# Kernel optimization log

Hardware: AMD Instinct MI355X
Metric: run time of the kernel (lower is better)

Reference implementation:

```python
import jax, jax.numpy as jnp
import numpy as np

EPS = 1e-5  # torch BatchNorm1d default eps


def setup_inputs() -> dict:
    key = jax.random.key(0)
    ks = jax.random.split(key, 4)
    B, D, H, T = 1024, 256, 1024, 128
    s_ih = 1.0 / np.sqrt(H)
    return {
        "x": jax.random.normal(ks[0], (B, D), dtype=jnp.float32),
        "h0": jnp.zeros((B, H), dtype=jnp.float32),
        "W_ih": jax.random.normal(ks[1], (3 * H, D), dtype=jnp.float32) * s_ih,
        "W_hh": jax.random.normal(ks[2], (3 * H, H), dtype=jnp.float32) * s_ih,
        "b_ih": jnp.zeros((3 * H,), dtype=jnp.float32),
        "b_hh": jnp.zeros((3 * H,), dtype=jnp.float32),
        "W_lin": jax.random.normal(ks[3], (D, H), dtype=jnp.float32) * s_ih,
        "b_lin": jnp.zeros((D,), dtype=jnp.float32),
        "n_frames": T,
    }


def reference(x, h0, W_ih, W_hh, b_ih, b_hh, W_lin, b_lin, n_frames):
    H = h0.shape[-1]

    def step(carry, _):
        h, inp = carry
        gi = inp @ W_ih.T + b_ih          # (B, 3H)
        gh = h @ W_hh.T + b_hh            # (B, 3H)
        i_r, i_z, i_n = jnp.split(gi, 3, axis=-1)
        h_r, h_z, h_n = jnp.split(gh, 3, axis=-1)
        r = jax.nn.sigmoid(i_r + h_r)
        z = jax.nn.sigmoid(i_z + h_z)
        n = jnp.tanh(i_n + r * h_n)
        h_new = (1.0 - z) * n + z * h
        out = h_new @ W_lin.T + b_lin     # (B, D) -> next input
        return (h_new, out), out

    _, outs = jax.lax.scan(step, (h0, x), None, length=n_frames)  # (T, B, D)

    # BatchNorm1d(affine=False), training mode: per-frame batch statistics
    mean = outs.mean(axis=1, keepdims=True)
    var = outs.var(axis=1, keepdims=True)  # biased variance, as torch BN uses
    return (outs - mean) * jax.lax.rsqrt(var + EPS)
```

## Files before the change

### kernel.cpp

```cpp
#include <hip/hip_runtime.h>


#define DEVI __device__ __forceinline__

typedef __bf16 bf16x8 __attribute__((ext_vector_type(8)));
typedef float f32x4 __attribute__((ext_vector_type(4)));
typedef unsigned int u32x4 __attribute__((ext_vector_type(4)));

typedef __attribute__((address_space(1))) const unsigned int g_u32;
typedef __attribute__((address_space(3))) unsigned int l_u32;

DEVI unsigned short f2b(float f) {
  union { float f; unsigned u; } v; v.f = f;
  return (unsigned short)((v.u + 0x7fffu + ((v.u >> 16) & 1u)) >> 16);
}

DEVI void gl_lds16(const void* g, void* s) {
  __builtin_amdgcn_global_load_lds((g_u32*)g, (l_u32*)s, 16, 0, 0);
}
DEVI void st16_sc1(void* p, u32x4 v) {
  asm volatile("global_store_dwordx4 %0, %1, off sc1"
               :: "v"((unsigned long long)(__SIZE_TYPE__)p), "v"(v) : "memory");
}

DEVI float sigm(float x) { return 1.0f / (1.0f + __expf(-x)); }
DEVI float tanh_f(float x) {
  float t = __expf(-2.0f * fabsf(x));
  float r = (1.0f - t) / (1.0f + t);
  return x >= 0.0f ? r : -r;
}

__global__ __launch_bounds__(256, 2) void gru_persist(
    const unsigned short* __restrict__ XB,
    const unsigned short* __restrict__ WP0,
    const unsigned short* __restrict__ WP,
    const float* __restrict__ C0v,
    const float* __restrict__ CBv,
    const float* __restrict__ h0,
    unsigned short* __restrict__ HH,
    unsigned int* __restrict__ bar)
{
  __shared__ __align__(16) unsigned short As[3][64 * 64];
  __shared__ __align__(16) unsigned short Bs[3][128 * 64];
  __shared__ __align__(16) unsigned short Hs[64 * 32];
  const int tid = threadIdx.x;
  const int w = tid >> 6, lane = tid & 63;
  const int wr = w >> 1, wc = w & 1;
  const int srow = lane >> 3;
  const int schunk = (lane & 7) ^ srow;
  const int l15 = lane & 15, lg = lane >> 4;
  const int xb_ = blockIdx.x & 7, rb_ = blockIdx.x >> 3;
  const int mb = (xb_ >> 2) | ((rb_ & 7) << 1);
  const int nb = (xb_ & 3) | ((rb_ >> 3) << 2);
  const int j = nb * 32 + wc * 16 + l15;

  const float c0r = C0v[j], c0z = C0v[1024 + j], c0i = C0v[2048 + j], c0h = C0v[3072 + j];
  const float cbr = CBv[j], cbz = CBv[1024 + j], cbi = CBv[2048 + j], cbh = CBv[3072 + j];

  float hreg[2][4];
#pragma unroll
  for (int mi = 0; mi < 2; ++mi)
#pragma unroll
    for (int i = 0; i < 4; ++i)
      hreg[mi][i] = h0[(size_t)(mb * 64 + wr * 32 + mi * 16 + lg * 4 + i) * 1024 + j];

  int offA[2][2], offB[2][4];
#pragma unroll
  for (int kk = 0; kk < 2; ++kk) {
#pragma unroll
    for (int mi = 0; mi < 2; ++mi) {
      int rl = wr * 32 + mi * 16 + l15;
      int slot = (kk * 4 + lg) ^ (rl & 7);
      offA[kk][mi] = rl * 128 + slot * 16;
    }
#pragma unroll
    for (int g = 0; g < 4; ++g) {
      int cl = wc * 64 + g * 16 + l15;
      int slot = (kk * 4 + lg) ^ (cl & 7);
      offB[kk][g] = cl * 128 + slot * 16;
    }
  }
  const int offq0 = srow * 1024 + schunk * 8;
  const int offq1 = (8 + srow) * 1024 + schunk * 8;
  const int offq2 = (16 + srow) * 1024 + schunk * 8;
  const int offq3 = (24 + srow) * 1024 + schunk * 8;
  const size_t arow_off = (size_t)(mb * 64 + w * 16) * 1024;
  const unsigned short* BrowS = WP + (size_t)(nb * 128 + w * 32) * 1024;
  const unsigned short* Arow0 = XB + (size_t)(mb * 64 + w * 16) * 256;
  const unsigned short* Brow0 = WP0 + (size_t)(nb * 128 + w * 32) * 256;

#define STAGE0(KT, BUF)                                                       \
  _Pragma("unroll")                                                           \
  for (int q = 0; q < 4; ++q)                                                 \
    gl_lds16(Brow0 + (size_t)(q * 8 + srow) * 256 + (KT) * 64 + schunk * 8,   \
             (char*)Bs[BUF] + (w * 32 + q * 8) * 128);                        \
  _Pragma("unroll")                                                           \
  for (int q = 0; q < 2; ++q)                                                 \
    gl_lds16(Arow0 + (size_t)(q * 8 + srow) * 256 + (KT) * 64 + schunk * 8,   \
             (char*)As[BUF] + (w * 16 + q * 8) * 128);
#define SSTAGE_B(KT, BUF)                                                     \
  gl_lds16(BrowS + offq0 + (KT) * 64, (char*)Bs[BUF] + (w * 32) * 128);       \
  gl_lds16(BrowS + offq1 + (KT) * 64, (char*)Bs[BUF] + (w * 32 + 8) * 128);   \
  gl_lds16(BrowS + offq2 + (KT) * 64, (char*)Bs[BUF] + (w * 32 + 16) * 128);  \
  gl_lds16(BrowS + offq3 + (KT) * 64, (char*)Bs[BUF] + (w * 32 + 24) * 128);
#define SSTAGE_A(KT, BUF)                                                     \
  gl_lds16(ArowS + offq0 + (KT) * 64, (char*)As[BUF] + (w * 16) * 128);       \
  gl_lds16(ArowS + offq1 + (KT) * 64, (char*)As[BUF] + (w * 16 + 8) * 128);

  for (int t = 0; t < 128; ++t) {
    const bool first = (t == 0);
    const int iters = first ? 4 : 16;
    const unsigned short* ArowS =
        HH + (((size_t)(first ? 0 : t - 1)) << 20) + arow_off;

    f32x4 acc[2][4] = {};

    if (first) {
      STAGE0(0, 0)
      STAGE0(1, 1)
    } else {
      SSTAGE_A(0, 0)
      SSTAGE_A(1, 1)
    }
    int cur = 0, pre = 2;
    for (int kt = 0; kt < iters; ++kt) {
      if (kt == 0) {
        if (first) asm volatile("s_waitcnt vmcnt(6)" ::: "memory");
        else       asm volatile("s_waitcnt vmcnt(2)" ::: "memory");
      } else if (kt == iters - 1) {
        asm volatile("s_waitcnt vmcnt(0)" ::: "memory");
      } else {
        asm volatile("s_waitcnt vmcnt(6)" ::: "memory");
      }
      __builtin_amdgcn_s_barrier();
      if (kt + 2 < iters) {
        if (first) { STAGE0(kt + 2, pre) }
        else       { SSTAGE_B(kt + 2, pre) SSTAGE_A(kt + 2, pre) }
      }
      __builtin_amdgcn_s_setprio(1);
#pragma unroll
      for (int kk = 0; kk < 2; ++kk) {
        bf16x8 a[2], b[4];
        const char* Ab = (const char*)As[cur];
        const char* Bb = (const char*)Bs[cur];
#pragma unroll
        for (int mi = 0; mi < 2; ++mi)
          a[mi] = *(const bf16x8*)(Ab + offA[kk][mi]);
#pragma unroll
        for (int g = 0; g < 4; ++g)
          b[g] = *(const bf16x8*)(Bb + offB[kk][g]);
#pragma unroll
        for (int mi = 0; mi < 2; ++mi)
#pragma unroll
          for (int g = 0; g < 4; ++g)
            acc[mi][g] = __builtin_amdgcn_mfma_f32_16x16x32_bf16(
                a[mi], b[g], acc[mi][g], 0, 0, 0);
      }
      __builtin_amdgcn_s_setprio(0);
      cur = (cur == 2) ? 0 : cur + 1;
      pre = (pre == 2) ? 0 : pre + 1;
    }

    const float cr = first ? c0r : cbr, cz = first ? c0z : cbz;
    const float ci = first ? c0i : cbi, ch = first ? c0h : cbh;
#pragma unroll
    for (int mi = 0; mi < 2; ++mi)
#pragma unroll
      for (int i = 0; i < 4; ++i) {
        float rg = sigm(acc[mi][0][i] + cr);
        float zg = sigm(acc[mi][1][i] + cz);
        float ng = tanh_f(acc[mi][2][i] + ci + rg * (acc[mi][3][i] + ch));
        float h = (1.0f - zg) * ng + zg * hreg[mi][i];
        hreg[mi][i] = h;
        Hs[(wr * 32 + mi * 16 + lg * 4 + i) * 32 + wc * 16 + l15] = f2b(h);
      }
    __syncthreads();
    {
      const int row = tid >> 2, part = tid & 3;
      u32x4 v = *(const u32x4*)((char*)Hs + tid * 16);
      size_t off = (size_t)(mb * 64 + row) * 1024 + nb * 32 + part * 8;
      st16_sc1(HH + ((size_t)t << 20) + off, v);
    }

    if (t != 127) {
      SSTAGE_B(0, 0)
      SSTAGE_B(1, 1)
      asm volatile("s_waitcnt vmcnt(8)" ::: "memory");
      __syncthreads();
      if (tid == 0)
        __hip_atomic_store(&bar[mb * 32 + nb], (unsigned)(t + 1),
                           __ATOMIC_RELAXED, __HIP_MEMORY_SCOPE_AGENT);
      if (w == 0) {
        const unsigned tgt = (unsigned)(t + 1);
        for (;;) {
          unsigned v = __hip_atomic_load(&bar[mb * 32 + (lane & 31)],
                                         __ATOMIC_RELAXED,
                                         __HIP_MEMORY_SCOPE_AGENT);
          if (__all((int)(v >= tgt))) break;
          __builtin_amdgcn_s_sleep(1);
        }
      }
      __syncthreads();
    }
  }
#undef STAGE0
#undef SSTAGE_A
#undef SSTAGE_B
}

__global__ __launch_bounds__(256) void outgemm(
    const unsigned short* __restrict__ A,
    const unsigned short* __restrict__ Bw,
    const float* __restrict__ bias,
    float* __restrict__ out,
    float* __restrict__ sumv,
    float* __restrict__ sumsq)
{
  __shared__ __align__(16) unsigned short As[128 * 64];
  __shared__ __align__(16) unsigned short Bs[128 * 64];
  const int tid = threadIdx.x;
  const int w = tid >> 6, lane = tid & 63;
  const int srow = lane >> 3, schunk = (lane & 7) ^ srow;
  const int l15 = lane & 15, lg = lane >> 4;
  const int mb = blockIdx.x >> 1, nb = blockIdx.x & 1;
  const int wr = w >> 1, wc = w & 1;
  f32x4 acc[4][4] = {};
  const unsigned short* Ag = A + (size_t)(mb * 128 + w * 32) * 1024;
  const unsigned short* Bg = Bw + (size_t)(nb * 128 + w * 32) * 1024;
  for (int kt = 0; kt < 16; ++kt) {
    const int k0 = kt * 64;
    __syncthreads();
#pragma unroll
    for (int q = 0; q < 4; ++q) {
      gl_lds16(Ag + (size_t)(q * 8 + srow) * 1024 + k0 + schunk * 8,
               (char*)As + (w * 32 + q * 8) * 128);
      gl_lds16(Bg + (size_t)(q * 8 + srow) * 1024 + k0 + schunk * 8,
               (char*)Bs + (w * 32 + q * 8) * 128);
    }
    __syncthreads();
#pragma unroll
    for (int kk = 0; kk < 2; ++kk) {
      bf16x8 a[4], b[4];
#pragma unroll
      for (int mi = 0; mi < 4; ++mi) {
        int rl = wr * 64 + mi * 16 + l15;
        int slot = (kk * 4 + lg) ^ (rl & 7);
        a[mi] = *(const bf16x8*)(As + rl * 64 + slot * 8);
      }
#pragma unroll
      for (int g = 0; g < 4; ++g) {
        int cl = g * 32 + wc * 16 + l15;
        int slot = (kk * 4 + lg) ^ (cl & 7);
        b[g] = *(const bf16x8*)(Bs + cl * 64 + slot * 8);
      }
#pragma unroll
      for (int mi = 0; mi < 4; ++mi)
#pragma unroll
        for (int g = 0; g < 4; ++g)
          acc[mi][g] = __builtin_amdgcn_mfma_f32_16x16x32_bf16(
              a[mi], b[g], acc[mi][g], 0, 0, 0);
    }
  }
  const int tf = mb >> 3;
  float s[4] = {0, 0, 0, 0}, ss[4] = {0, 0, 0, 0};
#pragma unroll
  for (int mi = 0; mi < 4; ++mi)
#pragma unroll
    for (int g = 0; g < 4; ++g) {
      int d = nb * 128 + g * 32 + wc * 16 + l15;
      float bb = bias[d];
#pragma unroll
      for (int i = 0; i < 4; ++i) {
        int row = mb * 128 + wr * 64 + mi * 16 + lg * 4 + i;
        float v = acc[mi][g][i] + bb;
        out[(size_t)row * 256 + d] = v;
        s[g] += v; ss[g] += v * v;
      }
    }
#pragma unroll
  for (int g = 0; g < 4; ++g) {
    s[g] += __shfl_xor(s[g], 16);  s[g] += __shfl_xor(s[g], 32);
    ss[g] += __shfl_xor(ss[g], 16); ss[g] += __shfl_xor(ss[g], 32);
  }
  if (lg == 0) {
#pragma unroll
    for (int g = 0; g < 4; ++g) {
      int d = nb * 128 + g * 32 + wc * 16 + l15;
      atomicAdd(&sumv[tf * 256 + d], s[g]);
      atomicAdd(&sumsq[tf * 256 + d], ss[g]);
    }
  }
}

__global__ __launch_bounds__(256) void gemm128(
    const unsigned short* __restrict__ A, const unsigned short* __restrict__ B,
    float* __restrict__ C, int K, int nT)
{
  __shared__ __align__(16) unsigned short As[128 * 64];
  __shared__ __align__(16) unsigned short Bs[128 * 64];
  const int tid = threadIdx.x;
  const int w = tid >> 6, lane = tid & 63;
  const int srow = lane >> 3, schunk = (lane & 7) ^ srow;
  const int l15 = lane & 15, lg = lane >> 4;
  const int mb = blockIdx.x / nT, nb = blockIdx.x % nT;
  const int wr = w >> 1, wc = w & 1;
  const int N = nT * 128;
  f32x4 acc[4][4] = {};
  const unsigned short* Ag = A + (size_t)(mb * 128 + w * 32) * K;
  const unsigned short* Bg = B + (size_t)(nb * 128 + w * 32) * K;
  for (int kt = 0; kt < (K >> 6); ++kt) {
    const int k0 = kt * 64;
    __syncthreads();
#pragma unroll
    for (int q = 0; q < 4; ++q) {
      gl_lds16(Ag + (size_t)(q * 8 + srow) * K + k0 + schunk * 8,
               (char*)As + (w * 32 + q * 8) * 128);
      gl_lds16(Bg + (size_t)(q * 8 + srow) * K + k0 + schunk * 8,
               (char*)Bs + (w * 32 + q * 8) * 128);
    }
    __syncthreads();
#pragma unroll
    for (int kk = 0; kk < 2; ++kk) {
      bf16x8 a[4], b[4];
#pragma unroll
      for (int mi = 0; mi < 4; ++mi) {
        int rl = wr * 64 + mi * 16 + l15;
        int slot = (kk * 4 + lg) ^ (rl & 7);
        a[mi] = *(const bf16x8*)(As + rl * 64 + slot * 8);
      }
#pragma unroll
      for (int g = 0; g < 4; ++g) {
        int cl = g * 32 + wc * 16 + l15;
        int slot = (kk * 4 + lg) ^ (cl & 7);
        b[g] = *(const bf16x8*)(Bs + cl * 64 + slot * 8);
      }
#pragma unroll
      for (int mi = 0; mi < 4; ++mi)
#pragma unroll
        for (int g = 0; g < 4; ++g)
          acc[mi][g] = __builtin_amdgcn_mfma_f32_16x16x32_bf16(
              a[mi], b[g], acc[mi][g], 0, 0, 0);
    }
  }
#pragma unroll
  for (int mi = 0; mi < 4; ++mi)
#pragma unroll
    for (int g = 0; g < 4; ++g)
#pragma unroll
      for (int i = 0; i < 4; ++i)
        C[(size_t)(mb * 128 + wr * 64 + mi * 16 + lg * 4 + i) * N + nb * 128 +
          g * 32 + wc * 16 + l15] = acc[mi][g][i];
}

__global__ void castall(const float* __restrict__ x, const float* __restrict__ wih,
                        const float* __restrict__ wlin, unsigned short* __restrict__ xb,
                        unsigned short* __restrict__ wihb, unsigned short* __restrict__ wlb) {
  int i = blockIdx.x * 256 + threadIdx.x;
  if (i < 262144) { xb[i] = f2b(x[i]); wlb[i] = f2b(wlin[i]); }
  if (i < 786432) wihb[i] = f2b(wih[i]);
}

__global__ void tcast(const float* __restrict__ in, unsigned short* __restrict__ out) {
  __shared__ float t[32][33];
  int i0 = blockIdx.x * 32, d0 = blockIdx.y * 32;
  for (int r = threadIdx.y; r < 32; r += 8)
    t[r][threadIdx.x] = in[(size_t)(d0 + r) * 1024 + i0 + threadIdx.x];
  __syncthreads();
  for (int r = threadIdx.y; r < 32; r += 8)
    out[(size_t)(i0 + r) * 256 + d0 + threadIdx.x] = f2b(t[threadIdx.x][r]);
}

__global__ void asmWp(const float* __restrict__ CMT, const float* __restrict__ Whh,
                      unsigned short* __restrict__ Wp) {
  int col = blockIdx.x;
  int jt = col >> 7, L = col & 127;
  int ch = L >> 6, gate = (L >> 4) & 3, c0 = L & 15;
  int j = jt * 32 + ch * 16 + c0;
  const float* s1;
  const float* s2 = nullptr;
  if (gate == 0)      { s1 = CMT + (size_t)j * 1024;          s2 = Whh + (size_t)j * 1024; }
  else if (gate == 1) { s1 = CMT + (size_t)(1024 + j) * 1024; s2 = Whh + (size_t)(1024 + j) * 1024; }
  else if (gate == 2) { s1 = CMT + (size_t)(2048 + j) * 1024; }
  else                { s1 = Whh + (size_t)(2048 + j) * 1024; }
  unsigned short* dst = Wp + (size_t)col * 1024;
  for (int k = threadIdx.x; k < 1024; k += 256) {
    float v = s1[k] + (s2 ? s2[k] : 0.0f);
    dst[k] = f2b(v);
  }
}

__global__ void asmWp0(const float* __restrict__ Wih, unsigned short* __restrict__ Wp0) {
  int col = blockIdx.x;
  int jt = col >> 7, L = col & 127;
  int ch = L >> 6, gate = (L >> 4) & 3, c0 = L & 15;
  int j = jt * 32 + ch * 16 + c0;
  int d = threadIdx.x;
  float v = 0.0f;
  if (gate < 3) v = Wih[(size_t)(gate * 1024 + j) * 256 + d];
  Wp0[(size_t)col * 256 + d] = f2b(v);
}

__global__ void biask(const float* __restrict__ Wih, const float* __restrict__ bih,
                      const float* __restrict__ bhh, const float* __restrict__ blin,
                      float* __restrict__ cbig, float* __restrict__ c0) {
  int j = blockIdx.x * 256 + threadIdx.x;
  if (j >= 1024) return;
  float bli[3];
  for (int g = 0; g < 3; ++g) {
    int gg = g * 1024 + j;
    float s = bih[gg];
    const float* wrow = Wih + (size_t)gg * 256;
    for (int d = 0; d < 256; ++d) s += blin[d] * wrow[d];
    bli[g] = s;
  }
  cbig[j] = bli[0] + bhh[j];
  cbig[1024 + j] = bli[1] + bhh[1024 + j];
  cbig[2048 + j] = bli[2];
  cbig[3072 + j] = bhh[2048 + j];
  c0[j] = bih[j] + bhh[j];
  c0[1024 + j] = bih[1024 + j] + bhh[1024 + j];
  c0[2048 + j] = bih[2048 + j];
  c0[3072 + j] = bhh[2048 + j];
}

__global__ void bnfin(const float* __restrict__ sv, const float* __restrict__ sq,
                      float* __restrict__ mean, float* __restrict__ rstd) {
  int i = blockIdx.x * 256 + threadIdx.x;
  float m = sv[i] * (1.0f / 1024.0f);
  float var = sq[i] * (1.0f / 1024.0f) - m * m;
  mean[i] = m;
  rstd[i] = rsqrtf(var + 1e-5f);
}

__global__ void bnnorm(float* __restrict__ o, const float* __restrict__ mean,
                       const float* __restrict__ rstd) {
  size_t base = ((size_t)blockIdx.x * 256 + threadIdx.x) * 4;
  int t = (int)(base >> 18);
  int d = (int)(base & 255);
  float4 v = *(float4*)(o + base);
  const float* mp = mean + t * 256 + d;
  const float* rp = rstd + t * 256 + d;
  float4 r;
  r.x = (v.x - mp[0]) * rp[0];
  r.y = (v.y - mp[1]) * rp[1];
  r.z = (v.z - mp[2]) * rp[2];
  r.w = (v.w - mp[3]) * rp[3];
  *(float4*)(o + base) = r;
}

extern "C" void kernel_launch(void* const* d_in, const int* in_sizes, int n_in,
                              void* d_out, int out_size, void* d_ws, size_t ws_size,
                              hipStream_t stream) {
  (void)in_sizes; (void)n_in; (void)out_size; (void)ws_size;
  const float* x    = (const float*)d_in[0];
  const float* h0   = (const float*)d_in[1];
  const float* Wih  = (const float*)d_in[2];
  const float* Whh  = (const float*)d_in[3];
  const float* bih  = (const float*)d_in[4];
  const float* bhh  = (const float*)d_in[5];
  const float* Wlin = (const float*)d_in[6];
  const float* blin = (const float*)d_in[7];
  float* out = (float*)d_out;

  char* ws = (char*)d_ws;
  size_t off = 0;
  auto alloc = [&](size_t bytes) {
    char* p = ws + off;
    off += (bytes + 255) & ~(size_t)255;
    return p;
  };
  unsigned short* WP   = (unsigned short*)alloc(4096ull * 1024 * 2);
  unsigned short* WP0  = (unsigned short*)alloc(4096ull * 256 * 2);
  unsigned short* WIHB = (unsigned short*)alloc(3072ull * 256 * 2);
  unsigned short* WLT  = (unsigned short*)alloc(1024ull * 256 * 2);
  unsigned short* WLB  = (unsigned short*)alloc(256ull * 1024 * 2);
  unsigned short* XB   = (unsigned short*)alloc(1024ull * 256 * 2);
  float* CMT  = (float*)alloc(3072ull * 1024 * 4);
  float* CBIG = (float*)alloc(4096 * 4);
  float* C0   = (float*)alloc(4096 * 4);
  unsigned short* HH  = (unsigned short*)alloc(128ull * 1024 * 1024 * 2);
  float* SUMV = (float*)alloc(128 * 256 * 4);
  float* SUMSQ= (float*)alloc(128 * 256 * 4);
  float* MEAN = (float*)alloc(128 * 256 * 4);
  float* RSTD = (float*)alloc(128 * 256 * 4);
  unsigned int* BAR = (unsigned int*)alloc(4096);

  (void)hipMemsetAsync(BAR, 0, 4096, stream);
  (void)hipMemsetAsync(SUMV, 0, 2 * 128 * 256 * 4, stream);

  castall<<<3072, 256, 0, stream>>>(x, Wih, Wlin, XB, WIHB, WLB);
  tcast<<<dim3(32, 8), dim3(32, 8), 0, stream>>>(Wlin, WLT);
  gemm128<<<192, 256, 0, stream>>>(WIHB, WLT, CMT, 256, 8);
  asmWp<<<4096, 256, 0, stream>>>(CMT, Whh, WP);
  asmWp0<<<4096, 256, 0, stream>>>(Wih, WP0);
  biask<<<4, 256, 0, stream>>>(Wih, bih, bhh, blin, CBIG, C0);

  gru_persist<<<512, 256, 0, stream>>>(XB, WP0, WP, C0, CBIG, h0, HH, BAR);

  outgemm<<<2048, 256, 0, stream>>>(HH, WLB, blin, out, SUMV, SUMSQ);

  bnfin<<<128, 256, 0, stream>>>(SUMV, SUMSQ, MEAN, RSTD);
  bnnorm<<<32768, 256, 0, stream>>>(out, MEAN, RSTD);
}
```

Measured before the change: 1.963 ms.

## Load recurrent A operand directly into registers instead of staging through LDS

```diff
diff --git a/kernel.cpp b/kernel.cpp
--- a/kernel.cpp
+++ b/kernel.cpp
@@ -84,10 +84,10 @@
   const int offq1 = (8 + srow) * 1024 + schunk * 8;
   const int offq2 = (16 + srow) * 1024 + schunk * 8;
   const int offq3 = (24 + srow) * 1024 + schunk * 8;
-  const size_t arow_off = (size_t)(mb * 64 + w * 16) * 1024;
   const unsigned short* BrowS = WP + (size_t)(nb * 128 + w * 32) * 1024;
   const unsigned short* Arow0 = XB + (size_t)(mb * 64 + w * 16) * 256;
   const unsigned short* Brow0 = WP0 + (size_t)(nb * 128 + w * 32) * 256;
+  const size_t aregrow = (size_t)(mb * 64 + wr * 32 + l15) * 1024 + lg * 8;
 
 #define STAGE0(KT, BUF)                                                       \
   _Pragma("unroll")                                                           \
@@ -103,64 +103,95 @@
   gl_lds16(BrowS + offq1 + (KT) * 64, (char*)Bs[BUF] + (w * 32 + 8) * 128);   \
   gl_lds16(BrowS + offq2 + (KT) * 64, (char*)Bs[BUF] + (w * 32 + 16) * 128);  \
   gl_lds16(BrowS + offq3 + (KT) * 64, (char*)Bs[BUF] + (w * 32 + 24) * 128);
-#define SSTAGE_A(KT, BUF)                                                     \
-  gl_lds16(ArowS + offq0 + (KT) * 64, (char*)As[BUF] + (w * 16) * 128);       \
-  gl_lds16(ArowS + offq1 + (KT) * 64, (char*)As[BUF] + (w * 16 + 8) * 128);
+
+#define ALOAD(KT, X00, X01, X10, X11)                                         \
+  {                                                                           \
+    const unsigned short* q0 = pa0 + (KT) * 64;                               \
+    const unsigned short* q1 = pa1 + (KT) * 64;                               \
+    X00 = *(const bf16x8*)(q0);      X01 = *(const bf16x8*)(q1);              \
+    X10 = *(const bf16x8*)(q0 + 32); X11 = *(const bf16x8*)(q1 + 32);         \
+  }
+
+#define MFMA_REG(X00, X01, X10, X11)                                          \
+  __builtin_amdgcn_s_setprio(1);                                              \
+  {                                                                           \
+    const char* Bb = (const char*)Bs[cur];                                    \
+    _Pragma("unroll")                                                         \
+    for (int g = 0; g < 4; ++g) {                                             \
+      bf16x8 b = *(const bf16x8*)(Bb + offB[0][g]);                           \
+      acc[0][g] = __builtin_amdgcn_mfma_f32_16x16x32_bf16(X00, b, acc[0][g], 0, 0, 0); \
+      acc[1][g] = __builtin_amdgcn_mfma_f32_16x16x32_bf16(X01, b, acc[1][g], 0, 0, 0); \
+    }                                                                         \
+    _Pragma("unroll")                                                         \
+    for (int g = 0; g < 4; ++g) {                                             \
+      bf16x8 b = *(const bf16x8*)(Bb + offB[1][g]);                           \
+      acc[0][g] = __builtin_amdgcn_mfma_f32_16x16x32_bf16(X10, b, acc[0][g], 0, 0, 0); \
+      acc[1][g] = __builtin_amdgcn_mfma_f32_16x16x32_bf16(X11, b, acc[1][g], 0, 0, 0); \
+    }                                                                         \
+  }                                                                           \
+  __builtin_amdgcn_s_setprio(0);
+
+#define RING_ADV  cur = (cur == 2) ? 0 : cur + 1; pre = (pre == 2) ? 0 : pre + 1;
 
   for (int t = 0; t < 128; ++t) {
-    const bool first = (t == 0);
-    const int iters = first ? 4 : 16;
-    const unsigned short* ArowS =
-        HH + (((size_t)(first ? 0 : t - 1)) << 20) + arow_off;
-
     f32x4 acc[2][4] = {};
-
-    if (first) {
+    int cur = 0, pre = 2;
+
+    if (t == 0) {
       STAGE0(0, 0)
       STAGE0(1, 1)
+      for (int kt = 0; kt < 4; ++kt) {
+        if (kt < 3) asm volatile("s_waitcnt vmcnt(6)" ::: "memory");
+        else        asm volatile("s_waitcnt vmcnt(0)" ::: "memory");
+        __builtin_amdgcn_s_barrier();
+        if (kt + 2 < 4) { STAGE0(kt + 2, pre) }
+        __builtin_amdgcn_s_setprio(1);
+#pragma unroll
+        for (int kk = 0; kk < 2; ++kk) {
+          bf16x8 a[2], b[4];
+          const char* Ab = (const char*)As[cur];
+          const char* Bb = (const char*)Bs[cur];
+#pragma unroll
+          for (int mi = 0; mi < 2; ++mi) a[mi] = *(const bf16x8*)(Ab + offA[kk][mi]);
+#pragma unroll
+          for (int g = 0; g < 4; ++g) b[g] = *(const bf16x8*)(Bb + offB[kk][g]);
+#pragma unroll
+          for (int mi = 0; mi < 2; ++mi)
+#pragma unroll
+            for (int g = 0; g < 4; ++g)
+              acc[mi][g] = __builtin_amdgcn_mfma_f32_16x16x32_bf16(
+                  a[mi], b[g], acc[mi][g], 0, 0, 0);
+        }
+        __builtin_amdgcn_s_setprio(0);
+        RING_ADV
+      }
     } else {
-      SSTAGE_A(0, 0)
-      SSTAGE_A(1, 1)
-    }
-    int cur = 0, pre = 2;
-    for (int kt = 0; kt < iters; ++kt) {
-      if (kt == 0) {
-        if (first) asm volatile("s_waitcnt vmcnt(6)" ::: "memory");
-        else       asm volatile("s_waitcnt vmcnt(2)" ::: "memory");
-      } else if (kt == iters - 1) {
-        asm volatile("s_waitcnt vmcnt(0)" ::: "memory");
-      } else {
-        asm volatile("s_waitcnt vmcnt(6)" ::: "memory");
-      }
-      __builtin_amdgcn_s_barrier();
-      if (kt + 2 < iters) {
-        if (first) { STAGE0(kt + 2, pre) }
-        else       { SSTAGE_B(kt + 2, pre) SSTAGE_A(kt + 2, pre) }
-      }
-      __builtin_amdgcn_s_setprio(1);
-#pragma unroll
-      for (int kk = 0; kk < 2; ++kk) {
-        bf16x8 a[2], b[4];
-        const char* Ab = (const char*)As[cur];
-        const char* Bb = (const char*)Bs[cur];
-#pragma unroll
-        for (int mi = 0; mi < 2; ++mi)
-          a[mi] = *(const bf16x8*)(Ab + offA[kk][mi]);
-#pragma unroll
-        for (int g = 0; g < 4; ++g)
-          b[g] = *(const bf16x8*)(Bb + offB[kk][g]);
-#pragma unroll
-        for (int mi = 0; mi < 2; ++mi)
-#pragma unroll
-          for (int g = 0; g < 4; ++g)
-            acc[mi][g] = __builtin_amdgcn_mfma_f32_16x16x32_bf16(
-                a[mi], b[g], acc[mi][g], 0, 0, 0);
-      }
-      __builtin_amdgcn_s_setprio(0);
-      cur = (cur == 2) ? 0 : cur + 1;
-      pre = (pre == 2) ? 0 : pre + 1;
-    }
-
+      const unsigned short* pa0 = HH + (((size_t)(t - 1)) << 20) + aregrow;
+      const unsigned short* pa1 = pa0 + 16 * 1024;
+      bf16x8 aA00, aA01, aA10, aA11, aB00, aB01, aB10, aB11;
+      ALOAD(0, aA00, aA01, aA10, aA11)
+      for (int kt2 = 0; kt2 < 8; ++kt2) {
+        const int e = kt2 * 2, o = e + 1;
+        asm volatile("s_waitcnt vmcnt(8)" ::: "memory");
+        __builtin_amdgcn_s_barrier();
+        if (e + 2 < 16) { SSTAGE_B(e + 2, pre) }
+        ALOAD(o, aB00, aB01, aB10, aB11)
+        if (e < 14) asm volatile("s_waitcnt vmcnt(8)" ::: "memory");
+        else        asm volatile("s_waitcnt vmcnt(4)" ::: "memory");
+        MFMA_REG(aA00, aA01, aA10, aA11)
+        RING_ADV
+        asm volatile("s_waitcnt vmcnt(8)" ::: "memory");
+        __builtin_amdgcn_s_barrier();
+        if (o + 2 < 16) { SSTAGE_B(o + 2, pre) }
+        if (o + 1 < 16) { ALOAD(o + 1, aA00, aA01, aA10, aA11) }
+        if (o < 15) asm volatile("s_waitcnt vmcnt(8)" ::: "memory");
+        else        asm volatile("s_waitcnt vmcnt(0)" ::: "memory");
+        MFMA_REG(aB00, aB01, aB10, aB11)
+        RING_ADV
+      }
+    }
+
+    const bool first = (t == 0);
     const float cr = first ? c0r : cbr, cz = first ? c0z : cbz;
     const float ci = first ? c0i : cbi, ch = first ? c0h : cbh;
 #pragma unroll
@@ -204,8 +235,10 @@
     }
   }
 #undef STAGE0
-#undef SSTAGE_A
 #undef SSTAGE_B
+#undef ALOAD
+#undef MFMA_REG
+#undef RING_ADV
 }
 
 __global__ __launch_bounds__(256) void outgemm(
```

After: 3.554 ms. +81.1%, slower.

## Split K across warp pairs in persistent GRU kernel with LDS reduction

Applied to the files above, without the earlier changes.

```diff
diff --git a/kernel.cpp b/kernel.cpp
--- a/kernel.cpp
+++ b/kernel.cpp
@@ -40,45 +40,42 @@
     unsigned short* __restrict__ HH,
     unsigned int* __restrict__ bar)
 {
-  __shared__ __align__(16) unsigned short As[3][64 * 64];
-  __shared__ __align__(16) unsigned short Bs[3][128 * 64];
-  __shared__ __align__(16) unsigned short Hs[64 * 32];
+  __shared__ __align__(16) unsigned short smem[38912];
+  unsigned short* const Asb = smem;
+  unsigned short* const Bsb = smem + 12288;
+  unsigned short* const Hs  = smem + 36864;
+
   const int tid = threadIdx.x;
   const int w = tid >> 6, lane = tid & 63;
-  const int wr = w >> 1, wc = w & 1;
+  const int tw = w & 1, kh = w >> 1;
   const int srow = lane >> 3;
   const int schunk = (lane & 7) ^ srow;
   const int l15 = lane & 15, lg = lane >> 4;
   const int xb_ = blockIdx.x & 7, rb_ = blockIdx.x >> 3;
   const int mb = (xb_ >> 2) | ((rb_ & 7) << 1);
   const int nb = (xb_ & 3) | ((rb_ >> 3) << 2);
-  const int j = nb * 32 + wc * 16 + l15;
+  const int j = nb * 32 + tw * 16 + l15;
 
   const float c0r = C0v[j], c0z = C0v[1024 + j], c0i = C0v[2048 + j], c0h = C0v[3072 + j];
   const float cbr = CBv[j], cbz = CBv[1024 + j], cbi = CBv[2048 + j], cbh = CBv[3072 + j];
 
-  float hreg[2][4];
-#pragma unroll
-  for (int mi = 0; mi < 2; ++mi)
-#pragma unroll
-    for (int i = 0; i < 4; ++i)
-      hreg[mi][i] = h0[(size_t)(mb * 64 + wr * 32 + mi * 16 + lg * 4 + i) * 1024 + j];
-
-  int offA[2][2], offB[2][4];
-#pragma unroll
-  for (int kk = 0; kk < 2; ++kk) {
-#pragma unroll
-    for (int mi = 0; mi < 2; ++mi) {
-      int rl = wr * 32 + mi * 16 + l15;
-      int slot = (kk * 4 + lg) ^ (rl & 7);
-      offA[kk][mi] = rl * 128 + slot * 16;
-    }
-#pragma unroll
-    for (int g = 0; g < 4; ++g) {
-      int cl = wc * 64 + g * 16 + l15;
-      int slot = (kk * 4 + lg) ^ (cl & 7);
-      offB[kk][g] = cl * 128 + slot * 16;
-    }
+  float hreg[4][4];
+  if (kh == 0) {
+#pragma unroll
+    for (int mi = 0; mi < 4; ++mi)
+#pragma unroll
+      for (int i = 0; i < 4; ++i)
+        hreg[mi][i] =
+            h0[(size_t)(mb * 64 + mi * 16 + lg * 4 + i) * 1024 + j];
+  }
+
+  int offA[4], offB[4];
+#pragma unroll
+  for (int q = 0; q < 4; ++q) {
+    int rl = q * 16 + l15;
+    offA[q] = rl * 128 + (((kh << 2) | lg) ^ (rl & 7)) * 16;
+    int cl = tw * 64 + q * 16 + l15;
+    offB[q] = cl * 128 + (((kh << 2) | lg) ^ (cl & 7)) * 16;
   }
   const int offq0 = srow * 1024 + schunk * 8;
   const int offq1 = (8 + srow) * 1024 + schunk * 8;
@@ -88,24 +85,44 @@
   const unsigned short* BrowS = WP + (size_t)(nb * 128 + w * 32) * 1024;
   const unsigned short* Arow0 = XB + (size_t)(mb * 64 + w * 16) * 256;
   const unsigned short* Brow0 = WP0 + (size_t)(nb * 128 + w * 32) * 256;
+  float* const scr = (float*)smem + tw * 4096;
 
 #define STAGE0(KT, BUF)                                                       \
   _Pragma("unroll")                                                           \
   for (int q = 0; q < 4; ++q)                                                 \
     gl_lds16(Brow0 + (size_t)(q * 8 + srow) * 256 + (KT) * 64 + schunk * 8,   \
-             (char*)Bs[BUF] + (w * 32 + q * 8) * 128);                        \
+             (char*)Bsb + (BUF) * 16384 + (w * 32 + q * 8) * 128);            \
   _Pragma("unroll")                                                           \
   for (int q = 0; q < 2; ++q)                                                 \
     gl_lds16(Arow0 + (size_t)(q * 8 + srow) * 256 + (KT) * 64 + schunk * 8,   \
-             (char*)As[BUF] + (w * 16 + q * 8) * 128);
+             (char*)Asb + (BUF) * 8192 + (w * 16 + q * 8) * 128);
 #define SSTAGE_B(KT, BUF)                                                     \
-  gl_lds16(BrowS + offq0 + (KT) * 64, (char*)Bs[BUF] + (w * 32) * 128);       \
-  gl_lds16(BrowS + offq1 + (KT) * 64, (char*)Bs[BUF] + (w * 32 + 8) * 128);   \
-  gl_lds16(BrowS + offq2 + (KT) * 64, (char*)Bs[BUF] + (w * 32 + 16) * 128);  \
-  gl_lds16(BrowS + offq3 + (KT) * 64, (char*)Bs[BUF] + (w * 32 + 24) * 128);
+  gl_lds16(BrowS + offq0 + (KT) * 64, (char*)Bsb + (BUF) * 16384 + (w * 32) * 128);       \
+  gl_lds16(BrowS + offq1 + (KT) * 64, (char*)Bsb + (BUF) * 16384 + (w * 32 + 8) * 128);   \
+  gl_lds16(BrowS + offq2 + (KT) * 64, (char*)Bsb + (BUF) * 16384 + (w * 32 + 16) * 128);  \
+  gl_lds16(BrowS + offq3 + (KT) * 64, (char*)Bsb + (BUF) * 16384 + (w * 32 + 24) * 128);
 #define SSTAGE_A(KT, BUF)                                                     \
-  gl_lds16(ArowS + offq0 + (KT) * 64, (char*)As[BUF] + (w * 16) * 128);       \
-  gl_lds16(ArowS + offq1 + (KT) * 64, (char*)As[BUF] + (w * 16 + 8) * 128);
+  gl_lds16(ArowS + offq0 + (KT) * 64, (char*)Asb + (BUF) * 8192 + (w * 16) * 128);        \
+  gl_lds16(ArowS + offq1 + (KT) * 64, (char*)Asb + (BUF) * 8192 + (w * 16 + 8) * 128);
+
+#define MFMA_CLUSTER                                                          \
+  __builtin_amdgcn_s_setprio(1);                                              \
+  {                                                                           \
+    const char* Ab = (const char*)Asb + cur * 8192;                           \
+    const char* Bb = (const char*)Bsb + cur * 16384;                          \
+    bf16x8 a[4], b[4];                                                        \
+    _Pragma("unroll")                                                         \
+    for (int q = 0; q < 4; ++q) a[q] = *(const bf16x8*)(Ab + offA[q]);        \
+    _Pragma("unroll")                                                         \
+    for (int q = 0; q < 4; ++q) b[q] = *(const bf16x8*)(Bb + offB[q]);        \
+    _Pragma("unroll")                                                         \
+    for (int mi = 0; mi < 4; ++mi)                                            \
+      _Pragma("unroll")                                                       \
+      for (int g = 0; g < 4; ++g)                                             \
+        acc[mi][g] = __builtin_amdgcn_mfma_f32_16x16x32_bf16(                 \
+            a[mi], b[g], acc[mi][g], 0, 0, 0);                                \
+  }                                                                           \
+  __builtin_amdgcn_s_setprio(0);
 
   for (int t = 0; t < 128; ++t) {
     const bool first = (t == 0);
@@ -113,7 +130,7 @@
     const unsigned short* ArowS =
         HH + (((size_t)(first ? 0 : t - 1)) << 20) + arow_off;
 
-    f32x4 acc[2][4] = {};
+    f32x4 acc[4][4] = {};
 
     if (first) {
       STAGE0(0, 0)
@@ -137,43 +154,39 @@
         if (first) { STAGE0(kt + 2, pre) }
         else       { SSTAGE_B(kt + 2, pre) SSTAGE_A(kt + 2, pre) }
       }
-      __builtin_amdgcn_s_setprio(1);
-#pragma unroll
-      for (int kk = 0; kk < 2; ++kk) {
-        bf16x8 a[2], b[4];
-        const char* Ab = (const char*)As[cur];
-        const char* Bb = (const char*)Bs[cur];
-#pragma unroll
-        for (int mi = 0; mi < 2; ++mi)
-          a[mi] = *(const bf16x8*)(Ab + offA[kk][mi]);
-#pragma unroll
-        for (int g = 0; g < 4; ++g)
-          b[g] = *(const bf16x8*)(Bb + offB[kk][g]);
-#pragma unroll
-        for (int mi = 0; mi < 2; ++mi)
-#pragma unroll
-          for (int g = 0; g < 4; ++g)
-            acc[mi][g] = __builtin_amdgcn_mfma_f32_16x16x32_bf16(
-                a[mi], b[g], acc[mi][g], 0, 0, 0);
-      }
-      __builtin_amdgcn_s_setprio(0);
+      MFMA_CLUSTER
       cur = (cur == 2) ? 0 : cur + 1;
       pre = (pre == 2) ? 0 : pre + 1;
     }
 
-    const float cr = first ? c0r : cbr, cz = first ? c0z : cbz;
-    const float ci = first ? c0i : cbi, ch = first ? c0h : cbh;
-#pragma unroll
-    for (int mi = 0; mi < 2; ++mi)
-#pragma unroll
-      for (int i = 0; i < 4; ++i) {
-        float rg = sigm(acc[mi][0][i] + cr);
-        float zg = sigm(acc[mi][1][i] + cz);
-        float ng = tanh_f(acc[mi][2][i] + ci + rg * (acc[mi][3][i] + ch));
-        float h = (1.0f - zg) * ng + zg * hreg[mi][i];
-        hreg[mi][i] = h;
-        Hs[(wr * 32 + mi * 16 + lg * 4 + i) * 32 + wc * 16 + l15] = f2b(h);
-      }
+    __syncthreads();
+    if (kh == 1) {
+#pragma unroll
+      for (int mi = 0; mi < 4; ++mi)
+#pragma unroll
+        for (int g = 0; g < 4; ++g)
+          *(f32x4*)(scr + (mi * 4 + g) * 256 + lane * 4) = acc[mi][g];
+    }
+    __syncthreads();
+    if (kh == 0) {
+      const float cr = first ? c0r : cbr, cz = first ? c0z : cbz;
+      const float ci = first ? c0i : cbi, ch = first ? c0h : cbh;
+#pragma unroll
+      for (int mi = 0; mi < 4; ++mi) {
+#pragma unroll
+        for (int g = 0; g < 4; ++g)
+          acc[mi][g] += *(const f32x4*)(scr + (mi * 4 + g) * 256 + lane * 4);
+#pragma unroll
+        for (int i = 0; i < 4; ++i) {
+          float rg = sigm(acc[mi][0][i] + cr);
+          float zg = sigm(acc[mi][1][i] + cz);
+          float ng = tanh_f(acc[mi][2][i] + ci + rg * (acc[mi][3][i] + ch));
+          float h = (1.0f - zg) * ng + zg * hreg[mi][i];
+          hreg[mi][i] = h;
+          Hs[(mi * 16 + lg * 4 + i) * 32 + tw * 16 + l15] = f2b(h);
+        }
+      }
+    }
     __syncthreads();
     {
       const int row = tid >> 2, part = tid & 3;
@@ -206,6 +219,7 @@
 #undef STAGE0
 #undef SSTAGE_A
 #undef SSTAGE_B
+#undef MFMA_CLUSTER
 }
 
 __global__ __launch_bounds__(256) void outgemm(
```

Result: slower. 2.067 ms (+5.3%).
